# Performance work log

Hardware: AMD Instinct MI355X
Metric: run time of the kernel (lower is better)

Reference implementation:

```python
import jax, jax.numpy as jnp
import numpy as np

E = 200000
T = 1000000
D = 128          # embed_dim
NB = 20          # n_basis (use_sh=False -> SimpleMLPAngleExpansion)


def setup_inputs() -> dict:
    key = jax.random.key(0)
    ks = jax.random.split(key, 16)
    s = lambda fan_in: 1.0 / np.sqrt(fan_in)
    return {
        "edge_attr": jax.random.normal(ks[0], (E, D), dtype=jnp.float32),
        "three_body_indices": jax.random.randint(ks[1], (T, 3), 0, 50000),
        "three_body_edge_indices": jax.random.randint(ks[2], (T, 2), 0, E),
        "edge_vectors": jax.random.normal(ks[3], (E, 3), dtype=jnp.float32),
        # SimpleMLPAngleExpansion: (len_ij, len_ik, cos) -> n_basis via 2-layer MLP
        "A1": jax.random.uniform(ks[4], (3, NB), jnp.float32, -s(3), s(3)),
        "ab1": jnp.zeros((NB,), jnp.float32),
        "A2": jax.random.uniform(ks[5], (NB, NB), jnp.float32, -s(NB), s(NB)),
        "ab2": jnp.zeros((NB,), jnp.float32),
        # phi_3b: Linear(2D+NB, D) -> SiLU -> Linear(D, D)
        "W1": jax.random.uniform(ks[6], (2 * D + NB, D), jnp.float32, -s(2 * D + NB), s(2 * D + NB)),
        "b1": jnp.zeros((D,), jnp.float32),
        "W2": jax.random.uniform(ks[7], (D, D), jnp.float32, -s(D), s(D)),
        "b2": jnp.zeros((D,), jnp.float32),
        # update_edge: Linear(D, D)
        "Wu": jax.random.uniform(ks[8], (D, D), jnp.float32, -s(D), s(D)),
        "bu": jnp.zeros((D,), jnp.float32),
    }


def reference(edge_attr, three_body_indices, three_body_edge_indices, edge_vectors,
              A1, ab1, A2, ab2, W1, b1, W2, b2, Wu, bu):
    e_ij = three_body_edge_indices[:, 0]
    e_ik = three_body_edge_indices[:, 1]
    vec_ij = -edge_vectors[e_ij]          # (T, 3)
    vec_ik = -edge_vectors[e_ik]          # (T, 3)
    len_ij = jnp.clip(jnp.linalg.norm(vec_ij, axis=1, keepdims=True), 1e-6)
    len_ik = jnp.clip(jnp.linalg.norm(vec_ik, axis=1, keepdims=True), 1e-6)
    cos = jnp.clip(jnp.sum(vec_ij * vec_ik, axis=1, keepdims=True) / (len_ij * len_ik), -1.0, 1.0)
    # angle expansion (SimpleMLPAngleExpansion): small MLP on geometric scalars
    f = jnp.concatenate([len_ij, len_ik, cos], axis=-1)       # (T, 3)
    angle_feats = jax.nn.silu(f @ A1 + ab1) @ A2 + ab2         # (T, NB)
    h_3b = jnp.concatenate([edge_attr[e_ij], edge_attr[e_ik], angle_feats], axis=-1)  # (T, 2D+NB)
    m_ijk = jax.nn.silu(h_3b @ W1 + b1) @ W2 + b2              # (T, D)
    delta = jax.ops.segment_sum(m_ijk, e_ij, num_segments=edge_attr.shape[0])  # (E, D)
    return delta @ Wu + bu
```

## Files before the change

### kernel.cpp

```cpp
#include <hip/hip_runtime.h>
#include <stdint.h>

#define D_ 128
#define NB_ 20
#define SCAN_B 1024

typedef __bf16 bf16x8 __attribute__((ext_vector_type(8)));
typedef float f32x4 __attribute__((ext_vector_type(4)));
typedef float f32x2 __attribute__((ext_vector_type(2)));

__device__ __forceinline__ float silu_f(float x) {
  return x * __builtin_amdgcn_rcpf(1.0f + __expf(-x));
}
__device__ __forceinline__ f32x2 silu2(f32x2 x) {
  return (f32x2){silu_f(x.x), silu_f(x.y)};
}
__device__ __forceinline__ f32x2 fsplat(float x) { return (f32x2){x, x}; }

__device__ __forceinline__ float bf2f(unsigned short u) {
  return __uint_as_float(((unsigned int)u) << 16);
}
__device__ __forceinline__ unsigned short f2bf(float f) {
  unsigned int x = __float_as_uint(f);
  return (unsigned short)((x + 0x7fffu + ((x >> 16) & 1u)) >> 16);
}

__global__ __launch_bounds__(256) void prep_kernel(
    const float* __restrict__ A2, const float* __restrict__ ab2,
    const float* __restrict__ W1, const float* __restrict__ b1,
    const float* __restrict__ W2, const float* __restrict__ Wu,
    const float* __restrict__ b2,
    float* __restrict__ Mfold, float* __restrict__ b1p,
    unsigned short* __restrict__ W2uT, float* __restrict__ c2,
    unsigned short* __restrict__ W1T) {
  int tid = blockIdx.x * blockDim.x + threadIdx.x;
  if (tid < 21 * D_) {
    int r = tid >> 7, c = tid & (D_ - 1);
    if (r < NB_) {
      float acc = 0.f;
      for (int j = 0; j < NB_; ++j) acc += A2[r * NB_ + j] * W1[(2 * D_ + j) * D_ + c];
      Mfold[r * D_ + c] = acc;
    } else {
      float acc = b1[c];
      for (int j = 0; j < NB_; ++j) acc += ab2[j] * W1[(2 * D_ + j) * D_ + c];
      b1p[c] = acc;
    }
  } else if (tid < 2688 + 16384) {
    int i = tid - 2688;
    int n = i >> 7, k = i & 127;
    float acc = 0.f;
    for (int m = 0; m < D_; ++m) acc += W2[k * D_ + m] * Wu[m * D_ + n];
    W2uT[i] = f2bf(acc);
  } else if (tid < 19072 + 128) {
    int n = tid - 19072;
    float acc = 0.f;
    for (int m = 0; m < D_; ++m) acc += b2[m] * Wu[m * D_ + n];
    c2[n] = acc;
  } else if (tid < 19200 + 32768) {
    int i = tid - 19200;
    int r = i >> 7, k = i & 127;
    int half = r >> 7, n = r & 127;
    W1T[i] = f2bf(W1[(size_t)(half * 128 + k) * D_ + n]);
  }
}

__global__ __launch_bounds__(256) void pq_mfma(const float* __restrict__ edge_attr,
                                               const unsigned short* __restrict__ W1T,
                                               unsigned short* __restrict__ P,
                                               unsigned short* __restrict__ Q, int E) {
  const int lane = threadIdx.x & 63;
  const int wave = threadIdx.x >> 6;
  const int e0 = (blockIdx.x * 4 + wave) * 16;
  if (e0 >= E) return;
  const int row = lane & 15;
  const int quad = lane >> 4;
  int e = e0 + row; if (e >= E) e = E - 1;

  union { bf16x8 v; unsigned short u[8]; } afr[4];
  const float* arow = edge_attr + (size_t)e * D_ + quad * 8;
#pragma unroll
  for (int kt = 0; kt < 4; ++kt) {
    float4 f0 = *(const float4*)(arow + kt * 32);
    float4 f1 = *(const float4*)(arow + kt * 32 + 4);
    afr[kt].u[0] = f2bf(f0.x); afr[kt].u[1] = f2bf(f0.y);
    afr[kt].u[2] = f2bf(f0.z); afr[kt].u[3] = f2bf(f0.w);
    afr[kt].u[4] = f2bf(f1.x); afr[kt].u[5] = f2bf(f1.y);
    afr[kt].u[6] = f2bf(f1.z); afr[kt].u[7] = f2bf(f1.w);
  }
#pragma unroll
  for (int half = 0; half < 2; ++half) {
    unsigned short* Obase = half ? Q : P;
#pragma unroll
    for (int nt = 0; nt < 8; ++nt) {
      const unsigned short* wrow =
          W1T + ((size_t)(half * 128 + nt * 16 + row)) * 128 + quad * 8;
      f32x4 acc = {0.f, 0.f, 0.f, 0.f};
#pragma unroll
      for (int kt = 0; kt < 4; ++kt) {
        bf16x8 bfr = *(const bf16x8*)(wrow + kt * 32);
        acc = __builtin_amdgcn_mfma_f32_16x16x32_bf16(afr[kt].v, bfr, acc, 0, 0, 0);
      }
      int n = nt * 16 + row;
#pragma unroll
      for (int i = 0; i < 4; ++i) {
        int er = e0 + quad * 4 + i;
        if (er < E) Obase[(size_t)er * D_ + n] = f2bf(acc[i]);
      }
    }
  }
}

__global__ void hist_kernel(const int* __restrict__ tbe, int* __restrict__ cnt, int T_) {
  int t = blockIdx.x * blockDim.x + threadIdx.x;
  if (t < T_) atomicAdd(&cnt[((const int2*)tbe)[t].x], 1);
}

__global__ __launch_bounds__(SCAN_B) void scan1_kernel(const int* __restrict__ cnt,
                                                       int* __restrict__ pre,
                                                       int* __restrict__ bsum, int E) {
  __shared__ int lds[SCAN_B];
  int tid = threadIdx.x, i = blockIdx.x * SCAN_B + tid;
  int v = (i < E) ? cnt[i] : 0;
  lds[tid] = v;
  __syncthreads();
  for (int d = 1; d < SCAN_B; d <<= 1) {
    int add = (tid >= d) ? lds[tid - d] : 0;
    __syncthreads();
    lds[tid] += add;
    __syncthreads();
  }
  if (i < E) pre[i] = lds[tid] - v;
  if (tid == SCAN_B - 1) bsum[blockIdx.x] = lds[tid];
}

__global__ void scan2_kernel(int* __restrict__ bsum, int nb) {
  __shared__ int lds[256];
  int tid = threadIdx.x;
  int v = (tid < nb) ? bsum[tid] : 0;
  lds[tid] = v;
  __syncthreads();
  for (int d = 1; d < 256; d <<= 1) {
    int add = (tid >= d) ? lds[tid - d] : 0;
    __syncthreads();
    lds[tid] += add;
    __syncthreads();
  }
  if (tid < nb) bsum[tid] = lds[tid] - v;
}

__global__ __launch_bounds__(SCAN_B) void scan3_kernel(const int* __restrict__ pre,
                                                       const int* __restrict__ bsum,
                                                       int* __restrict__ offs,
                                                       int* __restrict__ cursor, int E, int T_) {
  int i = blockIdx.x * SCAN_B + threadIdx.x;
  if (i < E) {
    int o = pre[i] + bsum[blockIdx.x];
    offs[i] = o;
    cursor[i] = o;
  }
  if (i == 0) offs[E] = T_;
}

__global__ void scatter_kernel(const int* __restrict__ tbe, int* __restrict__ cursor,
                               const float* __restrict__ edge_vectors,
                               const float* __restrict__ A1, const float* __restrict__ ab1,
                               int* __restrict__ seik, float* __restrict__ gT, int T_) {
  int t = blockIdx.x * blockDim.x + threadIdx.x;
  if (t >= T_) return;
  int2 v = ((const int2*)tbe)[t];
  int pos = atomicAdd(&cursor[v.x], 1);
  seik[pos] = v.y;
  const float* vj = edge_vectors + 3 * (size_t)v.x;
  const float* vk = edge_vectors + 3 * (size_t)v.y;
  float jx = vj[0], jy = vj[1], jz = vj[2];
  float kx = vk[0], ky = vk[1], kz = vk[2];
  float lij = fmaxf(__builtin_amdgcn_sqrtf(jx * jx + jy * jy + jz * jz), 1e-6f);
  float lik = fmaxf(__builtin_amdgcn_sqrtf(kx * kx + ky * ky + kz * kz), 1e-6f);
  float cosv = (jx * kx + jy * ky + jz * kz) * __builtin_amdgcn_rcpf(lij * lik);
  cosv = fminf(fmaxf(cosv, -1.f), 1.f);
  union { float4 v4[5]; float f[NB_]; } gr;
#pragma unroll
  for (int k = 0; k < NB_; ++k)
    gr.f[k] = silu_f(lij * A1[k] + lik * A1[NB_ + k] + cosv * A1[2 * NB_ + k] + ab1[k]);
  float4* gp = (float4*)(gT + (size_t)pos * NB_);
#pragma unroll
  for (int i = 0; i < 5; ++i) gp[i] = gr.v4[i];
}

struct G5 { float4 a, b, c, d, e; };

__device__ __forceinline__ G5 loadG(const char* __restrict__ gc, int t) {
  const float4* p = (const float4*)(
      gc + 80u * (unsigned)__builtin_amdgcn_readfirstlane(t));
  G5 g;
  g.a = p[0]; g.b = p[1]; g.c = p[2]; g.d = p[3]; g.e = p[4];
  return g;
}

__device__ __forceinline__ void body_acc(f32x2& acc, const f32x2 base,
                                         const G5& G, ushort2 qq,
                                         const f32x2* __restrict__ m) {
  const float* Gf = (const float*)&G;
  f32x2 u = base + (f32x2){bf2f(qq.x), bf2f(qq.y)};
  f32x2 ub = fsplat(0.f);
#pragma unroll
  for (int k = 0; k < NB_; k += 2) {
    u  += fsplat(Gf[k])     * m[k];
    ub += fsplat(Gf[k + 1]) * m[k + 1];
  }
  u += ub;
  acc += silu2(u);
}

__global__ __launch_bounds__(256, 4) void seg_kernel(
    const int* __restrict__ offs, const int* __restrict__ seik,
    const float* __restrict__ gT,
    const float* __restrict__ Mfold, const float* __restrict__ b1p,
    const unsigned short* __restrict__ P, const unsigned short* __restrict__ Q,
    float* __restrict__ s_out, int E) {
  const int lane = threadIdx.x & 63;
  const int wid = (blockIdx.x * blockDim.x + threadIdx.x) >> 6;
  const int nw = (gridDim.x * blockDim.x) >> 6;

  f32x2 m[NB_];
#pragma unroll
  for (int k = 0; k < NB_; ++k) {
    float2 t2 = *(const float2*)(Mfold + k * D_ + 2 * lane);
    m[k] = (f32x2){t2.x, t2.y};
  }
  const float2 bbt = *(const float2*)(b1p + 2 * lane);
  const f32x2 bb = (f32x2){bbt.x, bbt.y};

  const char* Qc = (const char*)Q;
  const char* Pc = (const char*)P;
  const char* gc = (const char*)gT;
  const unsigned loff = (unsigned)lane * 4u;

  int e = wid;
  if (e >= E) return;
  int o0 = offs[e], o1 = offs[e + 1];
  int eik0 = seik[__builtin_amdgcn_readfirstlane(o0)];
  ushort2 pp = *(const ushort2*)(Pc + ((unsigned)e << 8) + loff);

  for (; e < E; e += nw) {
    const int en = e + nw;
    int o0n = 0, o1n = 0, eik0n = 0;
    ushort2 ppn = make_ushort2(0, 0);
    if (en < E) {
      o0n = offs[en]; o1n = offs[en + 1];
      ppn = *(const ushort2*)(Pc + ((unsigned)en << 8) + loff);
      eik0n = seik[__builtin_amdgcn_readfirstlane(o0n)];
    }
    f32x2 acc = (f32x2){0.f, 0.f};
    if (o1 > o0) {
      const f32x2 base = (f32x2){bf2f(pp.x), bf2f(pp.y)} + bb;
      int t = o0;
      int eik_a = eik0;
      int eik_b = seik[__builtin_amdgcn_readfirstlane(o0 + 1)];
      int eik_c = seik[__builtin_amdgcn_readfirstlane(o0 + 2)];
      int eik_d = seik[__builtin_amdgcn_readfirstlane(o0 + 3)];
      ushort2 qq_a = *(const ushort2*)(Qc + ((unsigned)eik_a << 8) + loff);
      ushort2 qq_b = *(const ushort2*)(Qc + ((unsigned)eik_b << 8) + loff);
      G5 Ga = loadG(gc, t);
      G5 Gb;
      for (; t + 1 < o1; t += 2) {
        ushort2 qq_c = *(const ushort2*)(Qc + ((unsigned)eik_c << 8) + loff);
        Gb = loadG(gc, t + 1);
        int eik_e = seik[__builtin_amdgcn_readfirstlane(t + 4)];
        int eik_f = seik[__builtin_amdgcn_readfirstlane(t + 5)];
        body_acc(acc, base, Ga, qq_a, m);
        ushort2 qq_d = *(const ushort2*)(Qc + ((unsigned)eik_d << 8) + loff);
        Ga = loadG(gc, t + 2);
        body_acc(acc, base, Gb, qq_b, m);
        qq_a = qq_c; qq_b = qq_d;
        eik_c = eik_e; eik_d = eik_f;
      }
      if (t < o1) body_acc(acc, base, Ga, qq_a, m);
    }
    *(f32x2*)(s_out + (size_t)e * D_ + 2 * lane) = acc;
    o0 = o0n; o1 = o1n; pp = ppn; eik0 = eik0n;
  }
}

__global__ __launch_bounds__(256) void out_mfma(float* __restrict__ io,
                                                const unsigned short* __restrict__ W2uT,
                                                const float* __restrict__ c2,
                                                const float* __restrict__ bu,
                                                const int* __restrict__ cnt, int E) {
  const int lane = threadIdx.x & 63;
  const int wave = threadIdx.x >> 6;
  const int e0 = (blockIdx.x * 4 + wave) * 16;
  if (e0 >= E) return;
  const int row = lane & 15;
  const int quad = lane >> 4;
  int e = e0 + row; if (e >= E) e = E - 1;

  union { bf16x8 v; unsigned short u[8]; } afr[4];
  const float* arow = io + (size_t)e * D_ + quad * 8;
#pragma unroll
  for (int kt = 0; kt < 4; ++kt) {
    float4 f0 = *(const float4*)(arow + kt * 32);
    float4 f1 = *(const float4*)(arow + kt * 32 + 4);
    afr[kt].u[0] = f2bf(f0.x); afr[kt].u[1] = f2bf(f0.y);
    afr[kt].u[2] = f2bf(f0.z); afr[kt].u[3] = f2bf(f0.w);
    afr[kt].u[4] = f2bf(f1.x); afr[kt].u[5] = f2bf(f1.y);
    afr[kt].u[6] = f2bf(f1.z); afr[kt].u[7] = f2bf(f1.w);
  }
  float nf[4];
#pragma unroll
  for (int i = 0; i < 4; ++i) {
    int er = e0 + quad * 4 + i;
    nf[i] = (float)cnt[(er < E) ? er : (E - 1)];
  }
#pragma unroll
  for (int nt = 0; nt < 8; ++nt) {
    const unsigned short* wrow = W2uT + ((size_t)(nt * 16 + row)) * 128 + quad * 8;
    f32x4 acc = {0.f, 0.f, 0.f, 0.f};
#pragma unroll
    for (int kt = 0; kt < 4; ++kt) {
      bf16x8 bfr = *(const bf16x8*)(wrow + kt * 32);
      acc = __builtin_amdgcn_mfma_f32_16x16x32_bf16(afr[kt].v, bfr, acc, 0, 0, 0);
    }
    int n = nt * 16 + row;
    float c2n = c2[n], bun = bu[n];
#pragma unroll
    for (int i = 0; i < 4; ++i) {
      int er = e0 + quad * 4 + i;
      if (er < E) io[(size_t)er * D_ + n] = acc[i] + nf[i] * c2n + bun;
    }
  }
}

extern "C" void kernel_launch(void* const* d_in, const int* in_sizes, int n_in,
                              void* d_out, int out_size, void* d_ws, size_t ws_size,
                              hipStream_t stream) {
  const float* edge_attr    = (const float*)d_in[0];
  const int*   tbe          = (const int*)d_in[2];
  const float* edge_vectors = (const float*)d_in[3];
  const float* A1  = (const float*)d_in[4];
  const float* ab1 = (const float*)d_in[5];
  const float* A2  = (const float*)d_in[6];
  const float* ab2 = (const float*)d_in[7];
  const float* W1  = (const float*)d_in[8];
  const float* b1  = (const float*)d_in[9];
  const float* W2  = (const float*)d_in[10];
  const float* b2  = (const float*)d_in[11];
  const float* Wu  = (const float*)d_in[12];
  const float* bu  = (const float*)d_in[13];
  const int E = in_sizes[0] / D_;
  const int T = in_sizes[2] / 2;
  float* out = (float*)d_out;

  char* w = (char*)d_ws;
  auto carve = [&](size_t bytes) -> char* {
    char* p = w;
    w += (bytes + 255) & ~(size_t)255;
    return p;
  };
  unsigned short* P = (unsigned short*)carve((size_t)E * D_ * 2);
  unsigned short* Q = (unsigned short*)carve((size_t)E * D_ * 2);
  float* gT   = (float*)carve(((size_t)T + 8) * NB_ * 4);
  int* seik   = (int*)carve(((size_t)T + 8) * 4);
  int* cnt    = (int*)carve((size_t)E * 4);
  int* pre    = (int*)carve((size_t)E * 4);
  int* offs   = (int*)carve((size_t)(E + 1) * 4);
  int* cursor = (int*)carve((size_t)E * 4);
  int* bsum   = (int*)carve(1024 * 4);
  float* Mfold = (float*)carve(NB_ * D_ * 4);
  float* b1p   = (float*)carve(D_ * 4);
  unsigned short* W2uT = (unsigned short*)carve(D_ * D_ * 2);
  float* c2    = (float*)carve(D_ * 4);
  unsigned short* W1T = (unsigned short*)carve(256 * 128 * 2);

  const int nb_scan = (E + SCAN_B - 1) / SCAN_B;

  hipMemsetAsync(cnt, 0, (size_t)E * 4, stream);
  hipMemsetAsync(seik + T, 0, 8 * 4, stream);

  prep_kernel<<<(51968 + 255) / 256, 256, 0, stream>>>(A2, ab2, W1, b1, W2, Wu, b2,
                                                       Mfold, b1p, W2uT, c2, W1T);
  pq_mfma<<<(E + 63) / 64, 256, 0, stream>>>(edge_attr, W1T, P, Q, E);

  hist_kernel<<<(T + 255) / 256, 256, 0, stream>>>(tbe, cnt, T);
  scan1_kernel<<<nb_scan, SCAN_B, 0, stream>>>(cnt, pre, bsum, E);
  scan2_kernel<<<1, 256, 0, stream>>>(bsum, nb_scan);
  scan3_kernel<<<nb_scan, SCAN_B, 0, stream>>>(pre, bsum, offs, cursor, E, T);
  scatter_kernel<<<(T + 255) / 256, 256, 0, stream>>>(tbe, cursor, edge_vectors,
                                                      A1, ab1, seik, gT, T);

  seg_kernel<<<1024, 256, 0, stream>>>(offs, seik, gT, Mfold, b1p, P, Q, out, E);
  out_mfma<<<(E + 63) / 64, 256, 0, stream>>>(out, W2uT, c2, bu, cnt, E);
}
```

Baseline: 697.9 us.

## Balance segment kernel work by splitting triplets evenly across waves

Replaces the round-robin edge-per-wave assignment in the segment-sum kernel with a merge-path style partition: a new kernel maps each wave to a starting edge so every wave handles an equal share of the sorted triplets. Each wave then streams a contiguous triplet range, flushing accumulators at segment boundaries, with a deeper software-pipelined prefetch of seik and Q rows. The grid doubles and the occupancy hint rises from 4 to 6 blocks. This aims to remove load imbalance from variable segment lengths and per-edge loop startup costs, at the price of an extra small kernel and more branchy inner-loop boundary handling.

Result: no change. 695.0 us (-0.4%).

```diff
diff --git a/kernel.cpp b/kernel.cpp
--- a/kernel.cpp
+++ b/kernel.cpp
@@ -4,6 +4,8 @@
 #define D_ 128
 #define NB_ 20
 #define SCAN_B 1024
+#define SEG_BLOCKS 2048
+#define NWAVES (SEG_BLOCKS * 256 / 64)
 
 typedef __bf16 bf16x8 __attribute__((ext_vector_type(8)));
 typedef float f32x4 __attribute__((ext_vector_type(4)));
@@ -161,6 +163,18 @@
   if (i == 0) offs[E] = T_;
 }
 
+__global__ __launch_bounds__(256) void wfill_kernel(const int* __restrict__ offs,
+                                                    int* __restrict__ wstart,
+                                                    int E, int T_, int NW) {
+  int e = blockIdx.x * blockDim.x + threadIdx.x;
+  if (e >= E) return;
+  unsigned long long a = (unsigned long long)offs[e] * (unsigned long long)NW;
+  unsigned long long b = (unsigned long long)offs[e + 1] * (unsigned long long)NW;
+  int w_lo = (int)((a + T_ - 1) / (unsigned long long)T_);
+  int w_hi = (int)((b + T_ - 1) / (unsigned long long)T_);
+  for (int w = w_lo; w < w_hi; ++w) wstart[w] = e;
+}
+
 __global__ void scatter_kernel(const int* __restrict__ tbe, int* __restrict__ cursor,
                                const float* __restrict__ edge_vectors,
                                const float* __restrict__ A1, const float* __restrict__ ab1,
@@ -212,15 +226,17 @@
   acc += silu2(u);
 }
 
-__global__ __launch_bounds__(256, 4) void seg_kernel(
+__global__ __launch_bounds__(256, 6) void seg_kernel(
     const int* __restrict__ offs, const int* __restrict__ seik,
     const float* __restrict__ gT,
     const float* __restrict__ Mfold, const float* __restrict__ b1p,
     const unsigned short* __restrict__ P, const unsigned short* __restrict__ Q,
-    float* __restrict__ s_out, int E) {
+    const int* __restrict__ wstart,
+    float* __restrict__ s_out, int E, int NW) {
   const int lane = threadIdx.x & 63;
-  const int wid = (blockIdx.x * blockDim.x + threadIdx.x) >> 6;
-  const int nw = (gridDim.x * blockDim.x) >> 6;
+  const int w = __builtin_amdgcn_readfirstlane(
+      (int)((blockIdx.x * blockDim.x + threadIdx.x) >> 6));
+  if (w >= NW) return;
 
   f32x2 m[NB_];
 #pragma unroll
@@ -230,55 +246,75 @@
   }
   const float2 bbt = *(const float2*)(b1p + 2 * lane);
   const f32x2 bb = (f32x2){bbt.x, bbt.y};
+
+  int es = (w == 0) ? 0 : wstart[w];
+  int ee = (w == NW - 1) ? E : wstart[w + 1];
+  if (es >= ee) return;
 
   const char* Qc = (const char*)Q;
   const char* Pc = (const char*)P;
   const char* gc = (const char*)gT;
   const unsigned loff = (unsigned)lane * 4u;
 
-  int e = wid;
-  if (e >= E) return;
-  int o0 = offs[e], o1 = offs[e + 1];
-  int eik0 = seik[__builtin_amdgcn_readfirstlane(o0)];
+  int e = es;
+  int t = offs[es];
+  const int tend = offs[ee];
+  int nxt = offs[es + 1];
+
   ushort2 pp = *(const ushort2*)(Pc + ((unsigned)e << 8) + loff);
-
-  for (; e < E; e += nw) {
-    const int en = e + nw;
-    int o0n = 0, o1n = 0, eik0n = 0;
-    ushort2 ppn = make_ushort2(0, 0);
-    if (en < E) {
-      o0n = offs[en]; o1n = offs[en + 1];
-      ppn = *(const ushort2*)(Pc + ((unsigned)en << 8) + loff);
-      eik0n = seik[__builtin_amdgcn_readfirstlane(o0n)];
+  int epn = (e + 1 < E) ? e + 1 : E - 1;
+  ushort2 ppn = *(const ushort2*)(Pc + ((unsigned)epn << 8) + loff);
+  f32x2 base = (f32x2){bf2f(pp.x), bf2f(pp.y)} + bb;
+  f32x2 acc = (f32x2){0.f, 0.f};
+
+  if (t < tend) {
+    int ek0 = seik[t], ek1 = seik[t + 1], ek2 = seik[t + 2], ek3 = seik[t + 3];
+    ushort2 q0 = *(const ushort2*)(Qc + ((unsigned)ek0 << 8) + loff);
+    ushort2 q1 = *(const ushort2*)(Qc + ((unsigned)ek1 << 8) + loff);
+    ushort2 q2 = *(const ushort2*)(Qc + ((unsigned)ek2 << 8) + loff);
+    ushort2 q3 = *(const ushort2*)(Qc + ((unsigned)ek3 << 8) + loff);
+    int ekA = seik[t + 4], ekB = seik[t + 5], ekC = seik[t + 6], ekD = seik[t + 7];
+    G5 Ga = loadG(gc, t);
+    G5 Gb = loadG(gc, t + 1);
+
+    while (t < tend) {
+      while (t == nxt) {
+        *(f32x2*)(s_out + (size_t)e * D_ + 2 * lane) = acc;
+        acc = (f32x2){0.f, 0.f};
+        ++e;
+        nxt = offs[e + 1];
+        base = (f32x2){bf2f(ppn.x), bf2f(ppn.y)} + bb;
+        int ep = (e + 1 < E) ? e + 1 : E - 1;
+        ppn = *(const ushort2*)(Pc + ((unsigned)ep << 8) + loff);
+      }
+      body_acc(acc, base, Ga, q0, m);
+      q0 = q1; q1 = q2; q2 = q3;
+      q3 = *(const ushort2*)(Qc + ((unsigned)ekA << 8) + loff);
+      ekA = ekB; ekB = ekC; ekC = ekD; ekD = seik[t + 8];
+      Ga = loadG(gc, t + 2);
+      ++t;
+      if (t >= tend) break;
+      while (t == nxt) {
+        *(f32x2*)(s_out + (size_t)e * D_ + 2 * lane) = acc;
+        acc = (f32x2){0.f, 0.f};
+        ++e;
+        nxt = offs[e + 1];
+        base = (f32x2){bf2f(ppn.x), bf2f(ppn.y)} + bb;
+        int ep = (e + 1 < E) ? e + 1 : E - 1;
+        ppn = *(const ushort2*)(Pc + ((unsigned)ep << 8) + loff);
+      }
+      body_acc(acc, base, Gb, q0, m);
+      q0 = q1; q1 = q2; q2 = q3;
+      q3 = *(const ushort2*)(Qc + ((unsigned)ekA << 8) + loff);
+      ekA = ekB; ekB = ekC; ekC = ekD; ekD = seik[t + 8];
+      Gb = loadG(gc, t + 2);
+      ++t;
     }
-    f32x2 acc = (f32x2){0.f, 0.f};
-    if (o1 > o0) {
-      const f32x2 base = (f32x2){bf2f(pp.x), bf2f(pp.y)} + bb;
-      int t = o0;
-      int eik_a = eik0;
-      int eik_b = seik[__builtin_amdgcn_readfirstlane(o0 + 1)];
-      int eik_c = seik[__builtin_amdgcn_readfirstlane(o0 + 2)];
-      int eik_d = seik[__builtin_amdgcn_readfirstlane(o0 + 3)];
-      ushort2 qq_a = *(const ushort2*)(Qc + ((unsigned)eik_a << 8) + loff);
-      ushort2 qq_b = *(const ushort2*)(Qc + ((unsigned)eik_b << 8) + loff);
-      G5 Ga = loadG(gc, t);
-      G5 Gb;
-      for (; t + 1 < o1; t += 2) {
-        ushort2 qq_c = *(const ushort2*)(Qc + ((unsigned)eik_c << 8) + loff);
-        Gb = loadG(gc, t + 1);
-        int eik_e = seik[__builtin_amdgcn_readfirstlane(t + 4)];
-        int eik_f = seik[__builtin_amdgcn_readfirstlane(t + 5)];
-        body_acc(acc, base, Ga, qq_a, m);
-        ushort2 qq_d = *(const ushort2*)(Qc + ((unsigned)eik_d << 8) + loff);
-        Ga = loadG(gc, t + 2);
-        body_acc(acc, base, Gb, qq_b, m);
-        qq_a = qq_c; qq_b = qq_d;
-        eik_c = eik_e; eik_d = eik_f;
-      }
-      if (t < o1) body_acc(acc, base, Ga, qq_a, m);
-    }
+  }
+  while (e < ee) {
     *(f32x2*)(s_out + (size_t)e * D_ + 2 * lane) = acc;
-    o0 = o0n; o1 = o1n; pp = ppn; eik0 = eik0n;
+    acc = (f32x2){0.f, 0.f};
+    ++e;
   }
 }
 
@@ -366,6 +402,7 @@
   int* offs   = (int*)carve((size_t)(E + 1) * 4);
   int* cursor = (int*)carve((size_t)E * 4);
   int* bsum   = (int*)carve(1024 * 4);
+  int* wstart = (int*)carve((size_t)NWAVES * 4);
   float* Mfold = (float*)carve(NB_ * D_ * 4);
   float* b1p   = (float*)carve(D_ * 4);
   unsigned short* W2uT = (unsigned short*)carve(D_ * D_ * 2);
@@ -385,9 +422,11 @@
   scan1_kernel<<<nb_scan, SCAN_B, 0, stream>>>(cnt, pre, bsum, E);
   scan2_kernel<<<1, 256, 0, stream>>>(bsum, nb_scan);
   scan3_kernel<<<nb_scan, SCAN_B, 0, stream>>>(pre, bsum, offs, cursor, E, T);
+  wfill_kernel<<<(E + 255) / 256, 256, 0, stream>>>(offs, wstart, E, T, NWAVES);
   scatter_kernel<<<(T + 255) / 256, 256, 0, stream>>>(tbe, cursor, edge_vectors,
                                                       A1, ab1, seik, gT, T);
 
-  seg_kernel<<<1024, 256, 0, stream>>>(offs, seik, gT, Mfold, b1p, P, Q, out, E);
+  seg_kernel<<<SEG_BLOCKS, 256, 0, stream>>>(offs, seik, gT, Mfold, b1p, P, Q,
+                                             wstart, out, E, NWAVES);
   out_mfma<<<(E + 63) / 64, 256, 0, stream>>>(out, W2uT, c2, bu, cnt, E);
 }
```
